# Performance work log

Measured on AMD Instinct MI355X. Metric: run time of the kernel, lower is better.

## Reference

```python
import jax, jax.numpy as jnp
import numpy as np

N = 10000
E = 640000
IN_CH = 512
OUT_CH = 256
K = 2


def setup_inputs() -> dict:
    key = jax.random.key(0)
    k1, k2, k3, k4, k5 = jax.random.split(key, 5)
    x = jax.random.normal(k1, (N, IN_CH), dtype=jnp.float32)
    edge_index = jax.random.randint(k2, (2, E), 0, N, dtype=jnp.int64)
    lin_w = jax.random.normal(k3, (OUT_CH, IN_CH), dtype=jnp.float32) * (1.0 / np.sqrt(IN_CH))
    lin_b = jax.random.normal(k4, (OUT_CH,), dtype=jnp.float32) * 0.01
    weights = jax.random.uniform(k5, (K,), dtype=jnp.float32)
    return {"x": x, "edge_index": edge_index, "lin_w": lin_w, "lin_b": lin_b, "weights": weights}


def reference(x, edge_index, lin_w, lin_b, weights):
    n = x.shape[0]
    row, col = edge_index[0], edge_index[1]
    # deg = bincount(row); symmetric-normalized edge weights
    deg = jax.ops.segment_sum(jnp.ones(row.shape[0], dtype=x.dtype), row, num_segments=n)
    deg_inv_sqrt = jnp.where(deg > 0, jax.lax.rsqrt(deg), 0.0)
    norm = deg_inv_sqrt[row] * deg_inv_sqrt[col]  # [E]

    def spmm(h):
        # y[i] = sum_{e: row[e]==i} norm[e] * h[col[e]]
        return jax.ops.segment_sum(norm[:, None] * h[col], row, num_segments=n)

    out = x @ lin_w.T + lin_b  # [N, OUT_CH]
    # Faithful ARMA loop: x_k starts from the CURRENT accumulated `out` each hop-group
    for k in range(K):
        x_k = out
        for _ in range(k + 1):
            x_k = spmm(x_k)
        out = out + weights[k] * x_k
    return out
```

## Files before the change

kernel.cpp:

```cpp
#include <hip/hip_runtime.h>

#define N_NODES 10000
#define E_EDGES 640000
#define IN_CH   512
#define OUT_CH  256
#define HALF_CH 128
#define CSR_CAP (E_EDGES + 16 * N_NODES + 128)
#define G_GEMM_X 157
#define G_GEMM  (G_GEMM_X * 2)
#define G_SCAT  2500

typedef short bf16x8 __attribute__((ext_vector_type(8)));
typedef float f32x4  __attribute__((ext_vector_type(4)));

__device__ __forceinline__ unsigned short f2b(float f) {
    unsigned int u = __float_as_uint(f);
    return (unsigned short)((u + 0x7FFFu + ((u >> 16) & 1u)) >> 16);
}
__device__ __forceinline__ float lo16(unsigned int u) { return __uint_as_float(u << 16); }
__device__ __forceinline__ float hi16(unsigned int u) { return __uint_as_float(u & 0xFFFF0000u); }
__device__ __forceinline__ float b2f(unsigned short u) { return __uint_as_float(((unsigned int)u) << 16); }

__global__ void deg_kernel(const int* __restrict__ row, int* __restrict__ cursor32, int E) {
    int e = blockIdx.x * blockDim.x + threadIdx.x;
    if (e < E) atomicAdd(&cursor32[(row[e] << 5) + 1], 1);
}

__global__ void alloc_kernel(int* __restrict__ cursor32, int2* __restrict__ seg,
                             float* __restrict__ dinv, float* __restrict__ sq,
                             int* __restrict__ counter, int* __restrict__ csr_col, int n) {
    int i = blockIdx.x * blockDim.x + threadIdx.x;
    if (i >= n) return;
    int d = cursor32[(i << 5) + 1];
    dinv[i] = (d > 0) ? rsqrtf((float)d) : 0.0f;
    sq[i]   = (d > 0) ? sqrtf((float)d) : 0.0f;
    int pad = (d + 15) & ~15;
    int s = atomicAdd(counter, pad);
    seg[i] = make_int2(s, s + pad);
    cursor32[i << 5] = s;
    for (int j = d; j < pad; j++) csr_col[s + j] = N_NODES;
}

__global__ __launch_bounds__(256) void gemm_scatter(const float* __restrict__ x,
                                                    const float* __restrict__ w,
                                                    const float* __restrict__ bias,
                                                    const float* __restrict__ dinv,
                                                    unsigned short* __restrict__ h0b,
                                                    const int* __restrict__ row,
                                                    const int* __restrict__ col,
                                                    int* __restrict__ cursor32,
                                                    int* __restrict__ csr_col) {
    __shared__ unsigned short As[64][72];
    __shared__ unsigned short Bs[128][72];
    int bid = blockIdx.x;
    int tid = threadIdx.x;
    if (bid >= G_GEMM) {
        int e = (bid - G_GEMM) * 256 + tid;
        if (e < E_EDGES) {
            int r = row[e];
            int c = col[e];
            int p = atomicAdd(&cursor32[r << 5], 1);
            csr_col[p] = c;
        }
        return;
    }
    int bx = bid % G_GEMM_X;
    int plane = bid / G_GEMM_X;
    int wave = tid >> 6, lane = tid & 63, quad = lane >> 4, l16 = lane & 15;
    int row0 = bx * 64;
    int n0 = plane * 128;
    unsigned short* h0b_p = h0b + (size_t)plane * (N_NODES + 1) * HALF_CH;

    int ar = tid >> 2;
    int aseg = (tid & 3) * 16;
    int br = tid >> 1;
    int bseg = (tid & 1) * 32;

    f32x4 acc[8] = {};
    for (int k0 = 0; k0 < IN_CH; k0 += 64) {
        {
            int gr = row0 + ar;
            if (gr < N_NODES) {
                const float4* src = (const float4*)(x + (size_t)gr * IN_CH + k0 + aseg);
                #pragma unroll
                for (int i = 0; i < 4; i++) {
                    float4 v = src[i];
                    ushort4 o;
                    o.x = f2b(v.x); o.y = f2b(v.y); o.z = f2b(v.z); o.w = f2b(v.w);
                    *(ushort4*)&As[ar][aseg + i * 4] = o;
                }
            } else {
                ushort4 z = {0, 0, 0, 0};
                #pragma unroll
                for (int i = 0; i < 4; i++) *(ushort4*)&As[ar][aseg + i * 4] = z;
            }
        }
        {
            const float4* src = (const float4*)(w + (size_t)(n0 + br) * IN_CH + k0 + bseg);
            #pragma unroll
            for (int i = 0; i < 8; i++) {
                float4 v = src[i];
                ushort4 o;
                o.x = f2b(v.x); o.y = f2b(v.y); o.z = f2b(v.z); o.w = f2b(v.w);
                *(ushort4*)&Bs[br][bseg + i * 4] = o;
            }
        }
        __syncthreads();
        #pragma unroll
        for (int kk = 0; kk < 2; kk++) {
            bf16x8 a = *(const bf16x8*)&As[wave * 16 + l16][kk * 32 + quad * 8];
            #pragma unroll
            for (int t = 0; t < 8; t++) {
                bf16x8 b = *(const bf16x8*)&Bs[t * 16 + l16][kk * 32 + quad * 8];
                acc[t] = __builtin_amdgcn_mfma_f32_16x16x32_bf16(a, b, acc[t], 0, 0, 0);
            }
        }
        __syncthreads();
    }
    #pragma unroll
    for (int t = 0; t < 8; t++) {
        int lcol = t * 16 + l16;
        int col_ = n0 + lcol;
        float bv = bias[col_];
        #pragma unroll
        for (int r = 0; r < 4; r++) {
            int grow = row0 + wave * 16 + quad * 4 + r;
            if (grow < N_NODES) {
                float v = acc[t][r] + bv;
                h0b_p[(size_t)grow * HALF_CH + lcol] = f2b(v * dinv[grow]);
            }
        }
    }
    if (bx == 0 && tid < 64)
        ((unsigned int*)(h0b_p + (size_t)N_NODES * HALF_CH))[tid] = 0u;
}

__global__ __launch_bounds__(256) void spmm_kernel(const unsigned short* __restrict__ hb,
                                                   const int2* __restrict__ seg,
                                                   const int* __restrict__ csr_col,
                                                   const float* __restrict__ dinv,
                                                   const float* __restrict__ sq,
                                                   const unsigned short* __restrict__ prev_b,
                                                   const float* __restrict__ wts, int widx,
                                                   unsigned short* __restrict__ yb_out,
                                                   float* __restrict__ axpy_out,
                                                   unsigned short* __restrict__ axpyb_out,
                                                   int n) {
    int plane = blockIdx.x & 1;
    int node = (blockIdx.x >> 1) * 4 + (threadIdx.x >> 6);
    int lane = threadIdx.x & 63;
    if (node >= n) return;
    int sub = lane >> 4, l16 = lane & 15;
    size_t pstride = (size_t)(n + 1) * HALF_CH;
    const unsigned short* hp = hb + (size_t)plane * pstride;

    int2 se = seg[node];
    int s = se.x, e = se.y;
    float acc[8] = {0.f, 0.f, 0.f, 0.f, 0.f, 0.f, 0.f, 0.f};
    if (s < e) {
        int c0 = csr_col[s + 0  + sub];
        int c1 = csr_col[s + 4  + sub];
        int c2 = csr_col[s + 8  + sub];
        int c3 = csr_col[s + 12 + sub];
        int p = s;
        while (true) {
            int pn = p + 16;
            int n0c = csr_col[pn + 0  + sub];
            int n1c = csr_col[pn + 4  + sub];
            int n2c = csr_col[pn + 8  + sub];
            int n3c = csr_col[pn + 12 + sub];
            uint4 v0 = *(const uint4*)(hp + (size_t)c0 * HALF_CH + l16 * 8);
            uint4 v1 = *(const uint4*)(hp + (size_t)c1 * HALF_CH + l16 * 8);
            uint4 v2 = *(const uint4*)(hp + (size_t)c2 * HALF_CH + l16 * 8);
            uint4 v3 = *(const uint4*)(hp + (size_t)c3 * HALF_CH + l16 * 8);
            acc[0] += lo16(v0.x) + lo16(v1.x) + lo16(v2.x) + lo16(v3.x);
            acc[1] += hi16(v0.x) + hi16(v1.x) + hi16(v2.x) + hi16(v3.x);
            acc[2] += lo16(v0.y) + lo16(v1.y) + lo16(v2.y) + lo16(v3.y);
            acc[3] += hi16(v0.y) + hi16(v1.y) + hi16(v2.y) + hi16(v3.y);
            acc[4] += lo16(v0.z) + lo16(v1.z) + lo16(v2.z) + lo16(v3.z);
            acc[5] += hi16(v0.z) + hi16(v1.z) + hi16(v2.z) + hi16(v3.z);
            acc[6] += lo16(v0.w) + lo16(v1.w) + lo16(v2.w) + lo16(v3.w);
            acc[7] += hi16(v0.w) + hi16(v1.w) + hi16(v2.w) + hi16(v3.w);
            c0 = n0c; c1 = n1c; c2 = n2c; c3 = n3c; p = pn;
            if (p >= e) break;
        }
    }
    #pragma unroll
    for (int k = 0; k < 8; k++) {
        acc[k] += __shfl_xor(acc[k], 16, 64);
        acc[k] += __shfl_xor(acc[k], 32, 64);
    }
    if (sub != 0) return;

    float di = dinv[node];
    float y[8];
    #pragma unroll
    for (int k = 0; k < 8; k++) y[k] = di * acc[k];

    size_t pbase = (size_t)plane * pstride + (size_t)node * HALF_CH + l16 * 8;
    size_t padrow = (size_t)plane * pstride + (size_t)n * HALF_CH + l16 * 8;
    if (yb_out) {
        ushort4 o0, o1;
        o0.x = f2b(di * y[0]); o0.y = f2b(di * y[1]); o0.z = f2b(di * y[2]); o0.w = f2b(di * y[3]);
        o1.x = f2b(di * y[4]); o1.y = f2b(di * y[5]); o1.z = f2b(di * y[6]); o1.w = f2b(di * y[7]);
        *(ushort4*)(yb_out + pbase) = o0;
        *(ushort4*)(yb_out + pbase + 4) = o1;
        if (node == 0) {
            ushort4 z = {0, 0, 0, 0};
            *(ushort4*)(yb_out + padrow) = z;
            *(ushort4*)(yb_out + padrow + 4) = z;
        }
    }
    if (prev_b) {
        float wk = wts[widx];
        float sqn = sq[node];
        ushort4 p0 = *(const ushort4*)(prev_b + pbase);
        ushort4 p1 = *(const ushort4*)(prev_b + pbase + 4);
        float o[8];
        o[0] = b2f(p0.x) * sqn + wk * y[0];
        o[1] = b2f(p0.y) * sqn + wk * y[1];
        o[2] = b2f(p0.z) * sqn + wk * y[2];
        o[3] = b2f(p0.w) * sqn + wk * y[3];
        o[4] = b2f(p1.x) * sqn + wk * y[4];
        o[5] = b2f(p1.y) * sqn + wk * y[5];
        o[6] = b2f(p1.z) * sqn + wk * y[6];
        o[7] = b2f(p1.w) * sqn + wk * y[7];
        if (axpy_out) {
            size_t fbase = (size_t)node * OUT_CH + plane * HALF_CH + l16 * 8;
            float4 f0 = {o[0], o[1], o[2], o[3]};
            float4 f1 = {o[4], o[5], o[6], o[7]};
            *(float4*)(axpy_out + fbase) = f0;
            *(float4*)(axpy_out + fbase + 4) = f1;
        }
        if (axpyb_out) {
            ushort4 b0, b1;
            b0.x = f2b(di * o[0]); b0.y = f2b(di * o[1]); b0.z = f2b(di * o[2]); b0.w = f2b(di * o[3]);
            b1.x = f2b(di * o[4]); b1.y = f2b(di * o[5]); b1.z = f2b(di * o[6]); b1.w = f2b(di * o[7]);
            *(ushort4*)(axpyb_out + pbase) = b0;
            *(ushort4*)(axpyb_out + pbase + 4) = b1;
            if (node == 0) {
                ushort4 z = {0, 0, 0, 0};
                *(ushort4*)(axpyb_out + padrow) = z;
                *(ushort4*)(axpyb_out + padrow + 4) = z;
            }
        }
    }
}

extern "C" void kernel_launch(void* const* d_in, const int* in_sizes, int n_in,
                              void* d_out, int out_size, void* d_ws, size_t ws_size,
                              hipStream_t stream) {
    const float* x     = (const float*)d_in[0];
    const int*   ei    = (const int*)d_in[1];
    const float* lin_w = (const float*)d_in[2];
    const float* lin_b = (const float*)d_in[3];
    const float* wts   = (const float*)d_in[4];
    float* out = (float*)d_out;

    char* ws = (char*)d_ws;
    size_t off = 0;
    auto alloc = [&](size_t bytes) -> void* {
        void* p = ws + off;
        off += (bytes + 255) & ~(size_t)255;
        return p;
    };
    int*   cursor32 = (int*)  alloc(((size_t)N_NODES * 32 + 32) * 4);
    int*   counter  = cursor32 + (size_t)N_NODES * 32;
    int2*  seg      = (int2*) alloc((size_t)N_NODES * 8);
    float* dinv     = (float*)alloc(N_NODES * 4);
    float* sq       = (float*)alloc(N_NODES * 4);
    int*   csr_col  = (int*)  alloc((size_t)CSR_CAP * 4);
    unsigned short* h0b   = (unsigned short*)alloc((size_t)2 * (N_NODES + 1) * HALF_CH * 2);
    unsigned short* out1b = (unsigned short*)alloc((size_t)2 * (N_NODES + 1) * HALF_CH * 2);
    unsigned short* t2b   = (unsigned short*)alloc((size_t)2 * (N_NODES + 1) * HALF_CH * 2);

    hipMemsetAsync(cursor32, 0, ((size_t)N_NODES * 32 + 32) * 4, stream);

    const int* row = ei;
    const int* col = ei + E_EDGES;

    deg_kernel<<<(E_EDGES + 255) / 256, 256, 0, stream>>>(row, cursor32, E_EDGES);
    alloc_kernel<<<(N_NODES + 255) / 256, 256, 0, stream>>>(cursor32, seg, dinv, sq,
                                                            counter, csr_col, N_NODES);

    gemm_scatter<<<G_GEMM + G_SCAT, 256, 0, stream>>>(x, lin_w, lin_b, dinv, h0b,
                                                      row, col, cursor32, csr_col);

    int sgrid = 2 * ((N_NODES + 3) / 4);
    spmm_kernel<<<sgrid, 256, 0, stream>>>(h0b, seg, csr_col, dinv, sq, h0b,
                                           wts, 0, nullptr, nullptr, out1b, N_NODES);
    spmm_kernel<<<sgrid, 256, 0, stream>>>(out1b, seg, csr_col, dinv, sq, nullptr,
                                           wts, 0, t2b, nullptr, nullptr, N_NODES);
    spmm_kernel<<<sgrid, 256, 0, stream>>>(t2b, seg, csr_col, dinv, sq, out1b,
                                           wts, 1, nullptr, out, nullptr, N_NODES);
}
```

Before: 222.8 us.

## Fuse CSR build and GEMM into one cooperative kernel with per-XCC degree counters

Replaces the separate degree, allocation and scatter/GEMM kernels with one cooperative kernel that uses grid.sync between phases. Degree counts are kept in eight per-XCC planes to reduce cross-die atomic contention. The global atomic offset allocation is replaced by a deterministic block scan plus chunk-sum scan. This removes two kernel launches and the large padded cursor memset, but the GEMM now waits for the whole CSR build instead of running alongside the scatter, and it adds three grid-wide barriers.

Result: slower. 490.2 us (+120.0%).

```diff
diff --git a/kernel.cpp b/kernel.cpp
--- a/kernel.cpp
+++ b/kernel.cpp
@@ -1,14 +1,18 @@
 #include <hip/hip_runtime.h>
+#include <hip/hip_cooperative_groups.h>
+
+namespace cg = cooperative_groups;
 
 #define N_NODES 10000
 #define E_EDGES 640000
 #define IN_CH   512
 #define OUT_CH  256
 #define HALF_CH 128
+#define NPLANE  10240
+#define NCHUNK  40
 #define CSR_CAP (E_EDGES + 16 * N_NODES + 128)
 #define G_GEMM_X 157
 #define G_GEMM  (G_GEMM_X * 2)
-#define G_SCAT  2500
 
 typedef short bf16x8 __attribute__((ext_vector_type(8)));
 typedef float f32x4  __attribute__((ext_vector_type(4)));
@@ -21,49 +25,94 @@
 __device__ __forceinline__ float hi16(unsigned int u) { return __uint_as_float(u & 0xFFFF0000u); }
 __device__ __forceinline__ float b2f(unsigned short u) { return __uint_as_float(((unsigned int)u) << 16); }
 
-__global__ void deg_kernel(const int* __restrict__ row, int* __restrict__ cursor32, int E) {
-    int e = blockIdx.x * blockDim.x + threadIdx.x;
-    if (e < E) atomicAdd(&cursor32[(row[e] << 5) + 1], 1);
-}
-
-__global__ void alloc_kernel(int* __restrict__ cursor32, int2* __restrict__ seg,
-                             float* __restrict__ dinv, float* __restrict__ sq,
-                             int* __restrict__ counter, int* __restrict__ csr_col, int n) {
-    int i = blockIdx.x * blockDim.x + threadIdx.x;
-    if (i >= n) return;
-    int d = cursor32[(i << 5) + 1];
-    dinv[i] = (d > 0) ? rsqrtf((float)d) : 0.0f;
-    sq[i]   = (d > 0) ? sqrtf((float)d) : 0.0f;
-    int pad = (d + 15) & ~15;
-    int s = atomicAdd(counter, pad);
-    seg[i] = make_int2(s, s + pad);
-    cursor32[i << 5] = s;
-    for (int j = d; j < pad; j++) csr_col[s + j] = N_NODES;
-}
-
-__global__ __launch_bounds__(256) void gemm_scatter(const float* __restrict__ x,
-                                                    const float* __restrict__ w,
-                                                    const float* __restrict__ bias,
-                                                    const float* __restrict__ dinv,
-                                                    unsigned short* __restrict__ h0b,
-                                                    const int* __restrict__ row,
-                                                    const int* __restrict__ col,
-                                                    int* __restrict__ cursor32,
-                                                    int* __restrict__ csr_col) {
+__global__ __launch_bounds__(256) void fused_build_gemm(
+        const float* __restrict__ x,
+        const float* __restrict__ w,
+        const float* __restrict__ bias,
+        const int*   __restrict__ row,
+        const int*   __restrict__ col,
+        int*         __restrict__ cnt,
+        int*         __restrict__ rowstart,
+        int*         __restrict__ chunksum,
+        int2*        __restrict__ seg,
+        float*       __restrict__ dinv,
+        float*       __restrict__ sq,
+        int*         __restrict__ csr_col,
+        unsigned short* __restrict__ h0b) {
     __shared__ unsigned short As[64][72];
     __shared__ unsigned short Bs[128][72];
-    int bid = blockIdx.x;
-    int tid = threadIdx.x;
-    if (bid >= G_GEMM) {
-        int e = (bid - G_GEMM) * 256 + tid;
-        if (e < E_EDGES) {
-            int r = row[e];
-            int c = col[e];
-            int p = atomicAdd(&cursor32[r << 5], 1);
-            csr_col[p] = c;
-        }
-        return;
-    }
+    cg::grid_group grid = cg::this_grid();
+    const int tid = threadIdx.x;
+    const int bid = blockIdx.x;
+    const int gsz = gridDim.x * 256;
+
+    unsigned int xcc;
+    asm volatile("s_getreg_b32 %0, hwreg(HW_REG_XCC_ID)" : "=s"(xcc));
+    int* mycnt = cnt + (size_t)(xcc & 7) * NPLANE;
+
+    for (int e = bid * 256 + tid; e < E_EDGES; e += gsz)
+        atomicAdd(&mycnt[row[e]], 1);
+    grid.sync();
+
+    int* s_scan = (int*)&As[0][0];
+    if (bid < NCHUNK) {
+        int r = bid * 256 + tid;
+        int pad = 0;
+        if (r < N_NODES) {
+            int d = 0;
+            #pragma unroll
+            for (int p8 = 0; p8 < 8; p8++) d += cnt[p8 * NPLANE + r];
+            pad = (d + 15) & ~15;
+        }
+        s_scan[tid] = pad;
+        __syncthreads();
+        for (int off = 1; off < 256; off <<= 1) {
+            int v = (tid >= off) ? s_scan[tid - off] : 0;
+            __syncthreads();
+            s_scan[tid] += v;
+            __syncthreads();
+        }
+        if (r < N_NODES) rowstart[r] = s_scan[tid] - pad;
+        if (tid == 255) chunksum[bid] = s_scan[255];
+    }
+    grid.sync();
+
+    int* s_cb = (int*)&Bs[0][0];
+    if (tid < 64) {
+        int v = (tid < NCHUNK) ? chunksum[tid] : 0;
+        int inc = v;
+        #pragma unroll
+        for (int off = 1; off < 64; off <<= 1) {
+            int n = __shfl_up(inc, off, 64);
+            if (tid >= off) inc += n;
+        }
+        if (tid < NCHUNK) s_cb[tid] = inc - v;
+    }
+    __syncthreads();
+    for (int r = bid * 256 + tid; r < N_NODES; r += gsz) {
+        int c8[8], d = 0;
+        #pragma unroll
+        for (int p8 = 0; p8 < 8; p8++) { c8[p8] = cnt[p8 * NPLANE + r]; d += c8[p8]; }
+        int pad = (d + 15) & ~15;
+        int s = rowstart[r] + s_cb[r >> 8];
+        seg[r] = make_int2(s, s + pad);
+        int run = s;
+        #pragma unroll
+        for (int p8 = 0; p8 < 8; p8++) { cnt[p8 * NPLANE + r] = run; run += c8[p8]; }
+        dinv[r] = (d > 0) ? rsqrtf((float)d) : 0.0f;
+        sq[r]   = (d > 0) ? sqrtf((float)d) : 0.0f;
+        for (int j = d; j < pad; j++) csr_col[s + j] = N_NODES;
+    }
+    grid.sync();
+
+    for (int e = bid * 256 + tid; e < E_EDGES; e += gsz) {
+        int r = row[e];
+        int c = col[e];
+        int p = atomicAdd(&mycnt[r], 1);
+        csr_col[p] = c;
+    }
+
+    if (bid >= G_GEMM) return;
     int bx = bid % G_GEMM_X;
     int plane = bid / G_GEMM_X;
     int wave = tid >> 6, lane = tid & 63, quad = lane >> 4, l16 = lane & 15;
@@ -264,8 +313,9 @@
         off += (bytes + 255) & ~(size_t)255;
         return p;
     };
-    int*   cursor32 = (int*)  alloc(((size_t)N_NODES * 32 + 32) * 4);
-    int*   counter  = cursor32 + (size_t)N_NODES * 32;
+    int*   cnt      = (int*)  alloc((size_t)8 * NPLANE * 4);
+    int*   rowstart = (int*)  alloc((size_t)N_NODES * 4);
+    int*   chunksum = (int*)  alloc((size_t)NCHUNK * 4);
     int2*  seg      = (int2*) alloc((size_t)N_NODES * 8);
     float* dinv     = (float*)alloc(N_NODES * 4);
     float* sq       = (float*)alloc(N_NODES * 4);
@@ -274,17 +324,32 @@
     unsigned short* out1b = (unsigned short*)alloc((size_t)2 * (N_NODES + 1) * HALF_CH * 2);
     unsigned short* t2b   = (unsigned short*)alloc((size_t)2 * (N_NODES + 1) * HALF_CH * 2);
 
-    hipMemsetAsync(cursor32, 0, ((size_t)N_NODES * 32 + 32) * 4, stream);
+    hipMemsetAsync(cnt, 0, (size_t)8 * NPLANE * 4, stream);
 
     const int* row = ei;
     const int* col = ei + E_EDGES;
 
-    deg_kernel<<<(E_EDGES + 255) / 256, 256, 0, stream>>>(row, cursor32, E_EDGES);
-    alloc_kernel<<<(N_NODES + 255) / 256, 256, 0, stream>>>(cursor32, seg, dinv, sq,
-                                                            counter, csr_col, N_NODES);
-
-    gemm_scatter<<<G_GEMM + G_SCAT, 256, 0, stream>>>(x, lin_w, lin_b, dinv, h0b,
-                                                      row, col, cursor32, csr_col);
+    static int coopGrid = 0;
+    if (coopGrid == 0) {
+        int dev = 0;
+        hipGetDevice(&dev);
+        int numCU = 0;
+        hipDeviceGetAttribute(&numCU, hipDeviceAttributeMultiprocessorCount, dev);
+        int occ = 0;
+        hipOccupancyMaxActiveBlocksPerMultiprocessor(&occ, fused_build_gemm, 256, 0);
+        long g = (long)occ * (long)numCU;
+        if (g > 1280) g = 1280;
+        if (g < G_GEMM + NCHUNK) g = G_GEMM + NCHUNK;
+        coopGrid = (int)g;
+    }
+
+    void* kargs[] = {
+        (void*)&x, (void*)&lin_w, (void*)&lin_b, (void*)&row, (void*)&col,
+        (void*)&cnt, (void*)&rowstart, (void*)&chunksum,
+        (void*)&seg, (void*)&dinv, (void*)&sq, (void*)&csr_col, (void*)&h0b
+    };
+    hipLaunchCooperativeKernel((void*)fused_build_gemm, dim3(coopGrid), dim3(256),
+                               kargs, 0, stream);
 
     int sgrid = 2 * ((N_NODES + 3) / 4);
     spmm_kernel<<<sgrid, 256, 0, stream>>>(h0b, seg, csr_col, dinv, sq, h0b,
```

## Replace global-atomic CSR build with per-block LDS histogram and rank-based scatter

Applied to the files above, without the earlier changes.

Builds the CSR with a two-pass counting sort instead of global atomics. Each of 125 blocks takes a 5120-edge chunk, histograms row indices in a 10000-entry LDS array and records each edge's local rank. A per-row prefix over blocks then gives per-block base offsets, and the scatter writes csr_col deterministically without atomics. This removes the global atomic contention and the large cursor memset, but adds a 125x10000 count matrix that the per-row serial loops in alloc2 must walk, and puts only 125 scatter blocks alongside the GEMM.

Measured after the change: 200.2 us. 1.11x faster.

```diff
diff --git a/kernel.cpp b/kernel.cpp
--- a/kernel.cpp
+++ b/kernel.cpp
@@ -8,7 +8,8 @@
 #define CSR_CAP (E_EDGES + 16 * N_NODES + 128)
 #define G_GEMM_X 157
 #define G_GEMM  (G_GEMM_X * 2)
-#define G_SCAT  2500
+#define HBLK    125
+#define EPB     5120
 
 typedef short bf16x8 __attribute__((ext_vector_type(8)));
 typedef float f32x4  __attribute__((ext_vector_type(4)));
@@ -21,23 +22,43 @@
 __device__ __forceinline__ float hi16(unsigned int u) { return __uint_as_float(u & 0xFFFF0000u); }
 __device__ __forceinline__ float b2f(unsigned short u) { return __uint_as_float(((unsigned int)u) << 16); }
 
-__global__ void deg_kernel(const int* __restrict__ row, int* __restrict__ cursor32, int E) {
-    int e = blockIdx.x * blockDim.x + threadIdx.x;
-    if (e < E) atomicAdd(&cursor32[(row[e] << 5) + 1], 1);
-}
-
-__global__ void alloc_kernel(int* __restrict__ cursor32, int2* __restrict__ seg,
-                             float* __restrict__ dinv, float* __restrict__ sq,
-                             int* __restrict__ counter, int* __restrict__ csr_col, int n) {
-    int i = blockIdx.x * blockDim.x + threadIdx.x;
-    if (i >= n) return;
-    int d = cursor32[(i << 5) + 1];
-    dinv[i] = (d > 0) ? rsqrtf((float)d) : 0.0f;
-    sq[i]   = (d > 0) ? sqrtf((float)d) : 0.0f;
+__global__ __launch_bounds__(256) void hist_rank(const int* __restrict__ row,
+                                                 int* __restrict__ cnt,
+                                                 unsigned short* __restrict__ rank) {
+    __shared__ int hist[N_NODES];
+    int b = blockIdx.x, tid = threadIdx.x;
+    for (int i = tid; i < N_NODES; i += 256) hist[i] = 0;
+    __syncthreads();
+    int ebase = b * EPB;
+    #pragma unroll 4
+    for (int i = tid; i < EPB; i += 256) {
+        int r = row[ebase + i];
+        rank[ebase + i] = (unsigned short)atomicAdd(&hist[r], 1);
+    }
+    __syncthreads();
+    int* cb = cnt + (size_t)b * N_NODES;
+    for (int i = tid; i < N_NODES; i += 256) cb[i] = hist[i];
+}
+
+__global__ void alloc2(int* __restrict__ cnt,
+                       int2* __restrict__ seg,
+                       float* __restrict__ dinv, float* __restrict__ sq,
+                       int* __restrict__ counter, int* __restrict__ csr_col, int n) {
+    int r = blockIdx.x * blockDim.x + threadIdx.x;
+    if (r >= n) return;
+    int d = 0;
+    for (int b = 0; b < HBLK; b++) d += cnt[(size_t)b * N_NODES + r];
+    dinv[r] = (d > 0) ? rsqrtf((float)d) : 0.0f;
+    sq[r]   = (d > 0) ? sqrtf((float)d) : 0.0f;
     int pad = (d + 15) & ~15;
     int s = atomicAdd(counter, pad);
-    seg[i] = make_int2(s, s + pad);
-    cursor32[i << 5] = s;
+    seg[r] = make_int2(s, s + pad);
+    int run = s;
+    for (int b = 0; b < HBLK; b++) {
+        int c = cnt[(size_t)b * N_NODES + r];
+        cnt[(size_t)b * N_NODES + r] = run;
+        run += c;
+    }
     for (int j = d; j < pad; j++) csr_col[s + j] = N_NODES;
 }
 
@@ -48,19 +69,23 @@
                                                     unsigned short* __restrict__ h0b,
                                                     const int* __restrict__ row,
                                                     const int* __restrict__ col,
-                                                    int* __restrict__ cursor32,
+                                                    const int* __restrict__ base,
+                                                    const unsigned short* __restrict__ rank,
                                                     int* __restrict__ csr_col) {
     __shared__ unsigned short As[64][72];
     __shared__ unsigned short Bs[128][72];
     int bid = blockIdx.x;
     int tid = threadIdx.x;
     if (bid >= G_GEMM) {
-        int e = (bid - G_GEMM) * 256 + tid;
-        if (e < E_EDGES) {
+        int sb = bid - G_GEMM;
+        const int* bb = base + (size_t)sb * N_NODES;
+        int ebase = sb * EPB;
+        #pragma unroll 4
+        for (int i = tid; i < EPB; i += 256) {
+            int e = ebase + i;
             int r = row[e];
-            int c = col[e];
-            int p = atomicAdd(&cursor32[r << 5], 1);
-            csr_col[p] = c;
+            int p = bb[r] + (int)rank[e];
+            csr_col[p] = col[e];
         }
         return;
     }
@@ -264,8 +289,9 @@
         off += (bytes + 255) & ~(size_t)255;
         return p;
     };
-    int*   cursor32 = (int*)  alloc(((size_t)N_NODES * 32 + 32) * 4);
-    int*   counter  = cursor32 + (size_t)N_NODES * 32;
+    int*   cnt      = (int*)  alloc((size_t)HBLK * N_NODES * 4);
+    unsigned short* rank = (unsigned short*)alloc((size_t)E_EDGES * 2);
+    int*   counter  = (int*)  alloc(256);
     int2*  seg      = (int2*) alloc((size_t)N_NODES * 8);
     float* dinv     = (float*)alloc(N_NODES * 4);
     float* sq       = (float*)alloc(N_NODES * 4);
@@ -274,17 +300,17 @@
     unsigned short* out1b = (unsigned short*)alloc((size_t)2 * (N_NODES + 1) * HALF_CH * 2);
     unsigned short* t2b   = (unsigned short*)alloc((size_t)2 * (N_NODES + 1) * HALF_CH * 2);
 
-    hipMemsetAsync(cursor32, 0, ((size_t)N_NODES * 32 + 32) * 4, stream);
+    hipMemsetAsync(counter, 0, 4, stream);
 
     const int* row = ei;
     const int* col = ei + E_EDGES;
 
-    deg_kernel<<<(E_EDGES + 255) / 256, 256, 0, stream>>>(row, cursor32, E_EDGES);
-    alloc_kernel<<<(N_NODES + 255) / 256, 256, 0, stream>>>(cursor32, seg, dinv, sq,
-                                                            counter, csr_col, N_NODES);
-
-    gemm_scatter<<<G_GEMM + G_SCAT, 256, 0, stream>>>(x, lin_w, lin_b, dinv, h0b,
-                                                      row, col, cursor32, csr_col);
+    hist_rank<<<HBLK, 256, 0, stream>>>(row, cnt, rank);
+    alloc2<<<(N_NODES + 255) / 256, 256, 0, stream>>>(cnt, seg, dinv, sq,
+                                                      counter, csr_col, N_NODES);
+
+    gemm_scatter<<<G_GEMM + HBLK, 256, 0, stream>>>(x, lin_w, lin_b, dinv, h0b,
+                                                    row, col, cnt, rank, csr_col);
 
     int sgrid = 2 * ((N_NODES + 3) / 4);
     spmm_kernel<<<sgrid, 256, 0, stream>>>(h0b, seg, csr_col, dinv, sq, h0b,
```
